# Performance work log

Hardware: AMD Instinct MI355X
Metric: run time of the kernel (lower is better)

Reference implementation:

```python
import jax, jax.numpy as jnp
import numpy as np

B, D, E, H = 8192, 2048, 8, 128

def setup_inputs() -> dict:
    key = jax.random.key(0)
    ks = jax.random.split(key, 9)
    s_d = 1.0 / np.sqrt(D)
    s_h = 1.0 / np.sqrt(H)
    return {
        "x": jax.random.normal(ks[0], (B, D), dtype=jnp.float32),
        "gate_w": jax.random.normal(ks[1], (D, E), dtype=jnp.float32) * s_d,
        "gate_b": jnp.zeros((E,), dtype=jnp.float32),
        "W1": jax.random.normal(ks[2], (E, D, H), dtype=jnp.float32) * s_d,
        "b1": jnp.zeros((E, H), dtype=jnp.float32),
        "W2": jax.random.normal(ks[3], (E, H, H), dtype=jnp.float32) * s_h,
        "b2": jnp.zeros((E, H), dtype=jnp.float32),
        "W3": jax.random.normal(ks[4], (E, H, D), dtype=jnp.float32) * s_h,
        "b3": jnp.zeros((E, D), dtype=jnp.float32),
    }

def reference(x, gate_w, gate_b, W1, b1, W2, b2, W3, b3):
    # Adaptive gate: softmax over experts
    gates = jax.nn.softmax(x @ gate_w + gate_b, axis=1)          # [B, E]
    # All experts as one batched (grouped) GEMM over the expert axis.
    h1 = jax.nn.silu(jnp.einsum('bd,edh->ebh', x, W1) + b1[:, None, :])   # [E, B, H]
    h2 = jax.nn.silu(jnp.einsum('ebh,ehk->ebk', h1, W2) + b2[:, None, :]) # [E, B, H]
    y = jnp.einsum('ebh,ehd->ebd', h2, W3) + b3[:, None, :]               # [E, B, D]
    # Gate-weighted sum over experts (fused reduction, no [B,E,D] stack kept)
    out = jnp.einsum('be,ebd->bd', gates, y)                     # [B, D]
    return out
```

## Files before the change

kernel.cpp:

```cpp
#include <hip/hip_runtime.h>


typedef __attribute__((ext_vector_type(8))) short short8;
typedef __attribute__((ext_vector_type(4))) float f32x4;

#define B_SZ 8192
#define D_SZ 2048
#define E_SZ 8
#define H_SZ 128

#define VMCNT(n) asm volatile("s_waitcnt vmcnt(" #n ")" ::: "memory")
#define BAR()    __builtin_amdgcn_s_barrier()

__device__ __forceinline__ short f2bf(float f) {
  unsigned u = __builtin_bit_cast(unsigned, f);
  unsigned r = (u + 0x7fffu + ((u >> 16) & 1u)) >> 16;
  return (short)r;
}

__device__ __forceinline__ float silu_f(float v) {
  return v / (1.f + __expf(-v));
}

__device__ __forceinline__ void gload_lds16(const void* g, void* l) {
  __builtin_amdgcn_global_load_lds(
      (const __attribute__((address_space(1))) void*)g,
      (__attribute__((address_space(3))) void*)l,
      16, 0, 0);
}

__global__ __launch_bounds__(256)
void k_convert(const float* __restrict__ x,  const float* __restrict__ W1,
               const float* __restrict__ W2, const float* __restrict__ W3,
               short* __restrict__ xf, short* __restrict__ w1f,
               short* __restrict__ w2f, short* __restrict__ w3f)
{
  const int gi = blockIdx.x * 256 + threadIdx.x;
  if (gi < 2097152) {
    const int t = gi >> 10, r = gi & 1023;
    const int bt = t >> 5, kt = t & 31;
    const int kg = r >> 7, p = r & 127;
    const float* src = x + (size_t)(bt*128 + p)*2048 + kt*64 + kg*8;
    const float4 v0 = *(const float4*)src;
    const float4 v1 = *(const float4*)(src + 4);
    short8 o;
    o[0]=f2bf(v0.x); o[1]=f2bf(v0.y); o[2]=f2bf(v0.z); o[3]=f2bf(v0.w);
    o[4]=f2bf(v1.x); o[5]=f2bf(v1.y); o[6]=f2bf(v1.z); o[7]=f2bf(v1.w);
    *(short8*)(xf + (size_t)gi*8) = o;
  } else if (gi < 2097152 + 262144) {
    const int g = gi - 2097152;
    const int t = g >> 10, r = g & 1023;
    const int e = t >> 5, kt = t & 31;
    const int kg = r >> 7, p = r & 127;
    const int k0 = kt*64 + kg*8;
    short8 o;
    #pragma unroll
    for (int j = 0; j < 8; ++j)
      o[j] = f2bf(W1[(size_t)e*262144 + (size_t)(k0 + j)*128 + p]);
    *(short8*)(w1f + (size_t)g*8) = o;
  } else if (gi < 2097152 + 262144 + 16384) {
    const int g = gi - (2097152 + 262144);
    const int t = g >> 10, r = g & 1023;
    const int e = t >> 1, kt = t & 1;
    const int kg = r >> 7, p = r & 127;
    const int k0 = kt*64 + kg*8;
    short8 o;
    #pragma unroll
    for (int j = 0; j < 8; ++j)
      o[j] = f2bf(W2[(size_t)e*16384 + (size_t)(k0 + j)*128 + p]);
    *(short8*)(w2f + (size_t)g*8) = o;
  } else if (gi < 2637824) {
    const int g = gi - 2375680;
    const int t = g >> 10, r = g & 1023;
    const int nt = t >> 4, kt = t & 15;
    const int kg = r >> 7, p = r & 127;
    const int k0 = kt*64 + kg*8;
    short8 o;
    #pragma unroll
    for (int j = 0; j < 8; ++j) {
      const int k = k0 + j;
      o[j] = f2bf(W3[(size_t)(k >> 7)*262144 + (size_t)(k & 127)*2048 + nt*128 + p]);
    }
    *(short8*)(w3f + (size_t)g*8) = o;
  }
}

__global__ __launch_bounds__(256)
void k_gate(const float* __restrict__ x, const float* __restrict__ gw,
            const float* __restrict__ gb, float* __restrict__ gates)
{
  const int wid = threadIdx.x >> 6, lane = threadIdx.x & 63;
  const int row = blockIdx.x * 4 + wid;
  const float* xr = x + (size_t)row * 2048;
  float acc[8] = {0.f,0.f,0.f,0.f,0.f,0.f,0.f,0.f};
  for (int it = 0; it < 32; ++it) {
    const int k = it*64 + lane;
    const float xv = xr[k];
    const float4 g0 = *(const float4*)(gw + (size_t)k*8);
    const float4 g1 = *(const float4*)(gw + (size_t)k*8 + 4);
    acc[0] += xv*g0.x; acc[1] += xv*g0.y; acc[2] += xv*g0.z; acc[3] += xv*g0.w;
    acc[4] += xv*g1.x; acc[5] += xv*g1.y; acc[6] += xv*g1.z; acc[7] += xv*g1.w;
  }
  #pragma unroll
  for (int e = 0; e < 8; ++e) {
    #pragma unroll
    for (int d = 1; d < 64; d <<= 1)
      acc[e] += __shfl_xor(acc[e], d, 64);
  }
  if (lane == 0) {
    float lg[8], mx = -1e30f;
    #pragma unroll
    for (int e = 0; e < 8; ++e) { lg[e] = acc[e] + gb[e]; mx = fmaxf(mx, lg[e]); }
    float s = 0.f;
    #pragma unroll
    for (int e = 0; e < 8; ++e) { lg[e] = __expf(lg[e] - mx); s += lg[e]; }
    const float inv = 1.f / s;
    #pragma unroll
    for (int e = 0; e < 8; ++e) gates[(size_t)row*8 + e] = lg[e] * inv;
  }
}

__global__ __launch_bounds__(512, 2)
void k_gemm12(const short* __restrict__ xf, const short* __restrict__ w1f,
              const short* __restrict__ w2f,
              const float* __restrict__ b1, const float* __restrict__ b2,
              const float* __restrict__ gates, short* __restrict__ h2gf)
{
  __shared__ short lds[65536];
  const int wg = blockIdx.x;
  const int xcd = wg & 7, idx = wg >> 3;
  const int bt = xcd*8 + (idx >> 2);
  const int nt = idx & 3;

  const int tid  = threadIdx.x;
  const int lane = tid & 63;
  const int wid  = tid >> 6;
  const int wm = wid >> 2, wn = wid & 3;
  const int lm = lane & 15, lk = lane >> 4, lr = lane >> 4;
  const int wlds = (tid & ~63) * 8;

  const short* Ab  = xf + (size_t)bt*32*8192;
  const short* Bb0 = w1f + (size_t)(2*nt)*32*8192;
  const short* Bb1 = w1f + (size_t)(2*nt+1)*32*8192;

  f32x4 acc[4][4] = {};

  auto STAGE = [&](int n2) {
    const int tau = n2 >> 1, ks = n2 & 1, b = tau & 1;
    gload_lds16(Ab  + (size_t)tau*8192 + ks*4096 + tid*8,
                lds + b*24576 + ks*4096 + wlds);
    gload_lds16(Bb0 + (size_t)tau*8192 + ks*4096 + tid*8,
                lds + b*24576 + 8192 + ks*4096 + wlds);
    gload_lds16(Bb1 + (size_t)tau*8192 + ks*4096 + tid*8,
                lds + b*24576 + 16384 + ks*4096 + wlds);
  };

  STAGE(0); STAGE(1);
  VMCNT(3); BAR();

  for (int n = 0; n < 64; ++n) {
    const int tau = n >> 1, ks = n & 1, b = tau & 1;
    if (n + 2 < 64) STAGE(n + 2);
    short8 av[4], bv[4];
    #pragma unroll
    for (int f = 0; f < 4; ++f)
      av[f] = *(const short8*)(lds + b*24576 + (ks*4+lk)*1024 + (wm*64 + f*16 + lm)*8);
    #pragma unroll
    for (int f = 0; f < 4; ++f)
      bv[f] = *(const short8*)(lds + b*24576 + 8192 + (wn>>1)*8192 + (ks*4+lk)*1024
                               + ((wn&1)*64 + f*16 + lm)*8);
    #pragma unroll
    for (int i = 0; i < 4; ++i)
      #pragma unroll
      for (int j = 0; j < 4; ++j)
        acc[i][j] = __builtin_amdgcn_mfma_f32_16x16x32_bf16(av[i], bv[j], acc[i][j], 0, 0, 0);
    if (n + 2 < 64)      { VMCNT(3); BAR(); }
    else if (n + 1 < 64) { VMCNT(0); BAR(); }
  }
  BAR();

  #pragma unroll
  for (int q = 0; q < 8; ++q)
    gload_lds16(w2f + (size_t)nt*32768 + q*4096 + tid*8, lds + 32768 + q*4096 + wlds);

  float b1v[4];
  #pragma unroll
  for (int fn = 0; fn < 4; ++fn) b1v[fn] = b1[nt*256 + wn*64 + fn*16 + lm];
  #pragma unroll
  for (int fm = 0; fm < 4; ++fm)
  #pragma unroll
  for (int i = 0; i < 4; ++i) {
    const int m = wm*64 + fm*16 + lr*4 + i;
    #pragma unroll
    for (int fn = 0; fn < 4; ++fn) {
      const int n = wn*64 + fn*16 + lm;
      const float v = silu_f(acc[fm][fn][i] + b1v[fn]);
      lds[(n>>7)*16384 + ((n>>6)&1)*8192 + ((n>>3)&7)*1024 + m*8 + (n&7)] = f2bf(v);
    }
  }
  VMCNT(0); BAR();

  const int wm2 = wid >> 2, wn2 = wid & 3;
  #pragma unroll
  for (int eh = 0; eh < 2; ++eh) {
    f32x4 acc2[4][2] = {};
    #pragma unroll
    for (int kt2 = 0; kt2 < 2; ++kt2)
    #pragma unroll
    for (int ks = 0; ks < 2; ++ks) {
      short8 a2[4], b2v[2];
      #pragma unroll
      for (int f = 0; f < 4; ++f)
        a2[f] = *(const short8*)(lds + eh*16384 + kt2*8192 + (ks*4+lk)*1024
                                 + (wm2*64 + f*16 + lm)*8);
      #pragma unroll
      for (int f = 0; f < 2; ++f)
        b2v[f] = *(const short8*)(lds + 32768 + eh*16384 + kt2*8192 + (ks*4+lk)*1024
                                  + (wn2*32 + f*16 + lm)*8);
      #pragma unroll
      for (int i = 0; i < 4; ++i)
        #pragma unroll
        for (int j = 0; j < 2; ++j)
          acc2[i][j] = __builtin_amdgcn_mfma_f32_16x16x32_bf16(a2[i], b2v[j], acc2[i][j], 0, 0, 0);
    }
    BAR();

    const int e = 2*nt + eh;
    #pragma unroll
    for (int fm = 0; fm < 4; ++fm)
    #pragma unroll
    for (int i = 0; i < 4; ++i) {
      const int m = wm2*64 + fm*16 + lr*4 + i;
      const float g = gates[(size_t)(bt*128 + m)*8 + e];
      #pragma unroll
      for (int fn = 0; fn < 2; ++fn) {
        const int h = wn2*32 + fn*16 + lm;
        const float v = silu_f(acc2[fm][fn][i] + b2[e*128 + h]) * g;
        lds[32768 + ((h>>6)&1)*8192 + ((h>>3)&7)*1024 + m*8 + (h&7)] = f2bf(v);
      }
    }
    BAR();
    #pragma unroll
    for (int q = 0; q < 4; ++q) {
      const int li = q*4096 + tid*8;
      const int t2 = li >> 13, o = li & 8191;
      *(short8*)(h2gf + ((size_t)bt*16 + 2*e + t2)*8192 + o) =
          *(const short8*)(lds + 32768 + li);
    }
    if (eh == 0) BAR();
  }
}

__global__ __launch_bounds__(512, 2)
void k_gemm3(const short* __restrict__ h2gf, const short* __restrict__ w3f,
             const float* __restrict__ b3, const float* __restrict__ gates,
             float* __restrict__ out)
{
  __shared__ short lds[65536];
  const int wg = blockIdx.x;
  const int xcd = wg & 7, idx = wg >> 3;
  const int bt = xcd*4 + (idx & 3);
  const int nt = idx >> 2;

  const int tid  = threadIdx.x;
  const int lane = tid & 63;
  const int wid  = tid >> 6;
  const int wm = wid >> 2, wn = wid & 3;
  const int lm = lane & 15, lk = lane >> 4, lr = lane >> 4;
  const int wlds = (tid & ~63) * 8;

  const short* A0 = h2gf + (size_t)(bt*2)*16*8192;
  const short* A1 = h2gf + (size_t)(bt*2+1)*16*8192;
  const short* B0 = w3f + (size_t)(2*nt)*16*8192;
  const short* B1 = w3f + (size_t)(2*nt+1)*16*8192;

  f32x4 acc[8][4] = {};

  auto STAGE = [&](int n2) {
    const int tau = n2 >> 1, ks = n2 & 1, b = tau & 1;
    gload_lds16(A0 + (size_t)tau*8192 + ks*4096 + tid*8,
                lds + b*32768 + ks*4096 + wlds);
    gload_lds16(A1 + (size_t)tau*8192 + ks*4096 + tid*8,
                lds + b*32768 + 8192 + ks*4096 + wlds);
    gload_lds16(B0 + (size_t)tau*8192 + ks*4096 + tid*8,
                lds + b*32768 + 16384 + ks*4096 + wlds);
    gload_lds16(B1 + (size_t)tau*8192 + ks*4096 + tid*8,
                lds + b*32768 + 24576 + ks*4096 + wlds);
  };

  STAGE(0); STAGE(1);
  VMCNT(4); BAR();

  for (int n = 0; n < 32; ++n) {
    const int tau = n >> 1, ks = n & 1, b = tau & 1;
    if (n + 2 < 32) STAGE(n + 2);
    short8 av[8], bv[4];
    #pragma unroll
    for (int f = 0; f < 8; ++f)
      av[f] = *(const short8*)(lds + b*32768 + wm*8192 + (ks*4+lk)*1024 + (f*16 + lm)*8);
    #pragma unroll
    for (int f = 0; f < 4; ++f)
      bv[f] = *(const short8*)(lds + b*32768 + 16384 + (wn>>1)*8192 + (ks*4+lk)*1024
                               + ((wn&1)*64 + f*16 + lm)*8);
    #pragma unroll
    for (int i = 0; i < 8; ++i)
      #pragma unroll
      for (int j = 0; j < 4; ++j)
        acc[i][j] = __builtin_amdgcn_mfma_f32_16x16x32_bf16(av[i], bv[j], acc[i][j], 0, 0, 0);
    if (n + 2 < 32)      { VMCNT(4); BAR(); }
    else if (n + 1 < 32) { VMCNT(0); BAR(); }
  }

  float b3c[4][8];
  #pragma unroll
  for (int fn = 0; fn < 4; ++fn) {
    const int n = nt*256 + wn*64 + fn*16 + lm;
    #pragma unroll
    for (int e = 0; e < 8; ++e) b3c[fn][e] = b3[(size_t)e*D_SZ + n];
  }
  #pragma unroll
  for (int fm = 0; fm < 8; ++fm)
  #pragma unroll
  for (int i = 0; i < 4; ++i) {
    const int m = bt*256 + wm*128 + fm*16 + lr*4 + i;
    const float4 ga  = *(const float4*)(gates + (size_t)m*8);
    const float4 gbv = *(const float4*)(gates + (size_t)m*8 + 4);
    #pragma unroll
    for (int fn = 0; fn < 4; ++fn) {
      const int n = nt*256 + wn*64 + fn*16 + lm;
      const float bias = ga.x*b3c[fn][0] + ga.y*b3c[fn][1] + ga.z*b3c[fn][2] + ga.w*b3c[fn][3]
                       + gbv.x*b3c[fn][4] + gbv.y*b3c[fn][5] + gbv.z*b3c[fn][6] + gbv.w*b3c[fn][7];
      out[(size_t)m*D_SZ + n] = acc[fm][fn][i] + bias;
    }
  }
}

extern "C" void kernel_launch(void* const* d_in, const int* in_sizes, int n_in,
                              void* d_out, int out_size, void* d_ws, size_t ws_size,
                              hipStream_t stream)
{
  (void)in_sizes; (void)n_in; (void)out_size; (void)ws_size;
  const float* x  = (const float*)d_in[0];
  const float* gw = (const float*)d_in[1];
  const float* gb = (const float*)d_in[2];
  const float* W1 = (const float*)d_in[3];
  const float* b1 = (const float*)d_in[4];
  const float* W2 = (const float*)d_in[5];
  const float* b2 = (const float*)d_in[6];
  const float* W3 = (const float*)d_in[7];
  const float* b3 = (const float*)d_in[8];
  float* out = (float*)d_out;

  char* ws = (char*)d_ws;
  short* xf    = (short*)ws;  ws += (size_t)B_SZ*D_SZ*2;
  short* w1f   = (short*)ws;  ws += (size_t)E_SZ*D_SZ*H_SZ*2;
  short* w2f   = (short*)ws;  ws += (size_t)E_SZ*H_SZ*H_SZ*2;
  short* w3f   = (short*)ws;  ws += (size_t)E_SZ*H_SZ*D_SZ*2;
  float* gates = (float*)ws;  ws += (size_t)B_SZ*E_SZ*4;
  short* h2gf  = (short*)ws;  ws += (size_t)B_SZ*E_SZ*H_SZ*2;

  k_convert<<<dim3(10304), dim3(256), 0, stream>>>(x, W1, W2, W3, xf, w1f, w2f, w3f);
  k_gate   <<<dim3(2048),  dim3(256), 0, stream>>>(x, gw, gb, gates);
  k_gemm12 <<<dim3(256), dim3(512), 0, stream>>>(xf, w1f, w2f, b1, b2, gates, h2gf);
  k_gemm3  <<<dim3(256), dim3(512), 0, stream>>>(h2gf, w3f, b3, gates, out);
}
```

Measured before the change: 141.1 us.

## Split first GEMM into split-K 256x256 tiles and separate second-layer kernel

The fused GEMM1+GEMM2 kernel is replaced by a split-K GEMM1 kernel that uses a shared 256x256 tile core, writing two bf16 partial sums to a workspace. A new kernel then adds the partials, applies bias and SiLU, and runs the per-expert 128x128 GEMM2 with gating. The larger tile is meant to raise data reuse, and the split-K is meant to keep the grid at 256 blocks. In exchange it adds an extra launch and a round trip of partial sums through global memory, which also loses precision because the partials are rounded to bf16. MFMA sections are additionally wrapped in s_setprio.

After: 150.8 us. +6.9%, slower.

```diff
diff --git a/kernel.cpp b/kernel.cpp
--- a/kernel.cpp
+++ b/kernel.cpp
@@ -16,6 +16,10 @@
   unsigned u = __builtin_bit_cast(unsigned, f);
   unsigned r = (u + 0x7fffu + ((u >> 16) & 1u)) >> 16;
   return (short)r;
+}
+
+__device__ __forceinline__ float bf2f(short s) {
+  return __builtin_bit_cast(float, (unsigned)((unsigned short)s) << 16);
 }
 
 __device__ __forceinline__ float silu_f(float v) {
@@ -27,6 +31,58 @@
       (const __attribute__((address_space(1))) void*)g,
       (__attribute__((address_space(3))) void*)l,
       16, 0, 0);
+}
+
+template<int NKT>
+__device__ __forceinline__ void core256(const short* __restrict__ A0,
+                                        const short* __restrict__ A1,
+                                        const short* __restrict__ B0,
+                                        const short* __restrict__ B1,
+                                        short* lds, f32x4 acc[8][4])
+{
+  const int tid  = threadIdx.x;
+  const int lane = tid & 63;
+  const int wid  = tid >> 6;
+  const int wm = wid >> 2, wn = wid & 3;
+  const int lm = lane & 15, lk = lane >> 4;
+  const int wlds = (tid & ~63) * 8;
+
+  auto STAGE = [&](int n2) {
+    const int tau = n2 >> 1, ks = n2 & 1, b = tau & 1;
+    gload_lds16(A0 + (size_t)tau*8192 + ks*4096 + tid*8,
+                lds + b*32768 + ks*4096 + wlds);
+    gload_lds16(A1 + (size_t)tau*8192 + ks*4096 + tid*8,
+                lds + b*32768 + 8192 + ks*4096 + wlds);
+    gload_lds16(B0 + (size_t)tau*8192 + ks*4096 + tid*8,
+                lds + b*32768 + 16384 + ks*4096 + wlds);
+    gload_lds16(B1 + (size_t)tau*8192 + ks*4096 + tid*8,
+                lds + b*32768 + 24576 + ks*4096 + wlds);
+  };
+
+  STAGE(0); STAGE(1);
+  VMCNT(4); BAR();
+
+  for (int n = 0; n < 2*NKT; ++n) {
+    const int ks = n & 1, b = (n >> 1) & 1;
+    if (n + 2 < 2*NKT) STAGE(n + 2);
+    short8 av[8], bv[4];
+    #pragma unroll
+    for (int f = 0; f < 8; ++f)
+      av[f] = *(const short8*)(lds + b*32768 + wm*8192 + (ks*4+lk)*1024 + (f*16 + lm)*8);
+    #pragma unroll
+    for (int f = 0; f < 4; ++f)
+      bv[f] = *(const short8*)(lds + b*32768 + 16384 + (wn>>1)*8192 + (ks*4+lk)*1024
+                               + ((wn&1)*64 + f*16 + lm)*8);
+    __builtin_amdgcn_s_setprio(1);
+    #pragma unroll
+    for (int i = 0; i < 8; ++i)
+      #pragma unroll
+      for (int j = 0; j < 4; ++j)
+        acc[i][j] = __builtin_amdgcn_mfma_f32_16x16x32_bf16(av[i], bv[j], acc[i][j], 0, 0, 0);
+    __builtin_amdgcn_s_setprio(0);
+    if (n + 2 < 2*NKT)      { VMCNT(4); BAR(); }
+    else if (n + 1 < 2*NKT) { VMCNT(0); BAR(); }
+  }
 }
 
 __global__ __launch_bounds__(256)
@@ -121,133 +177,115 @@
 }
 
 __global__ __launch_bounds__(512, 2)
-void k_gemm12(const short* __restrict__ xf, const short* __restrict__ w1f,
-              const short* __restrict__ w2f,
+void k_gemm1s(const short* __restrict__ xf, const short* __restrict__ w1f,
+              short* __restrict__ p)
+{
+  __shared__ short lds[65536];
+  const int b = blockIdx.x;
+  const int xcd = b & 7, idx = b >> 3;
+  const int BT = xcd*4 + (idx >> 3);
+  const int rem = idx & 7;
+  const int NT = rem >> 1, kh = rem & 1;
+
+  f32x4 acc[8][4] = {};
+  core256<16>(xf  + ((size_t)(BT*2)  *32 + kh*16)*8192,
+              xf  + ((size_t)(BT*2+1)*32 + kh*16)*8192,
+              w1f + ((size_t)(2*NT)  *32 + kh*16)*8192,
+              w1f + ((size_t)(2*NT+1)*32 + kh*16)*8192,
+              lds, acc);
+
+  const int tid = threadIdx.x, lane = tid & 63, wid = tid >> 6;
+  const int wm = wid >> 2, wn = wid & 3, lm = lane & 15, lr = lane >> 4;
+  short* pd = p + (size_t)kh*8388608;
+  #pragma unroll
+  for (int fm = 0; fm < 8; ++fm)
+  #pragma unroll
+  for (int i = 0; i < 4; ++i) {
+    const int m = BT*256 + wm*128 + fm*16 + lr*4 + i;
+    #pragma unroll
+    for (int fn = 0; fn < 4; ++fn) {
+      const int n = NT*256 + wn*64 + fn*16 + lm;
+      pd[(size_t)m*1024 + n] = f2bf(acc[fm][fn][i]);
+    }
+  }
+}
+
+__global__ __launch_bounds__(256, 2)
+void k_gemm2m(const short* __restrict__ p, const short* __restrict__ w2f,
               const float* __restrict__ b1, const float* __restrict__ b2,
               const float* __restrict__ gates, short* __restrict__ h2gf)
 {
-  __shared__ short lds[65536];
-  const int wg = blockIdx.x;
-  const int xcd = wg & 7, idx = wg >> 3;
-  const int bt = xcd*8 + (idx >> 2);
-  const int nt = idx & 3;
-
-  const int tid  = threadIdx.x;
-  const int lane = tid & 63;
-  const int wid  = tid >> 6;
-  const int wm = wid >> 2, wn = wid & 3;
-  const int lm = lane & 15, lk = lane >> 4, lr = lane >> 4;
+  __shared__ short lds[32768];
+  const int bt2 = blockIdx.x, e = blockIdx.y;
+  const int tid = threadIdx.x;
   const int wlds = (tid & ~63) * 8;
 
-  const short* Ab  = xf + (size_t)bt*32*8192;
-  const short* Bb0 = w1f + (size_t)(2*nt)*32*8192;
-  const short* Bb1 = w1f + (size_t)(2*nt+1)*32*8192;
-
+  #pragma unroll
+  for (int q = 0; q < 8; ++q)
+    gload_lds16(w2f + (size_t)e*16384 + q*2048 + tid*8,
+                lds + 16384 + q*2048 + wlds);
+
+  #pragma unroll
+  for (int u = 0; u < 8; ++u) {
+    const int g = u*256 + tid;
+    const int m = g >> 4, hg = g & 15;
+    const size_t src = (size_t)(bt2*128 + m)*1024 + e*128 + hg*8;
+    const short8 a = *(const short8*)(p + src);
+    const short8 c = *(const short8*)(p + 8388608 + src);
+    short8 o;
+    #pragma unroll
+    for (int j = 0; j < 8; ++j) {
+      const float v = bf2f(a[j]) + bf2f(c[j]) + b1[e*128 + hg*8 + j];
+      o[j] = f2bf(silu_f(v));
+    }
+    *(short8*)(lds + (hg>>3)*8192 + (hg&7)*1024 + m*8) = o;
+  }
+  VMCNT(0);
+  __syncthreads();
+
+  const int lane = tid & 63, wid = tid >> 6;
+  const int wr = wid >> 1, wc = wid & 1, lm = lane & 15, lk = lane >> 4, lr = lane >> 4;
   f32x4 acc[4][4] = {};
-
-  auto STAGE = [&](int n2) {
-    const int tau = n2 >> 1, ks = n2 & 1, b = tau & 1;
-    gload_lds16(Ab  + (size_t)tau*8192 + ks*4096 + tid*8,
-                lds + b*24576 + ks*4096 + wlds);
-    gload_lds16(Bb0 + (size_t)tau*8192 + ks*4096 + tid*8,
-                lds + b*24576 + 8192 + ks*4096 + wlds);
-    gload_lds16(Bb1 + (size_t)tau*8192 + ks*4096 + tid*8,
-                lds + b*24576 + 16384 + ks*4096 + wlds);
-  };
-
-  STAGE(0); STAGE(1);
-  VMCNT(3); BAR();
-
-  for (int n = 0; n < 64; ++n) {
-    const int tau = n >> 1, ks = n & 1, b = tau & 1;
-    if (n + 2 < 64) STAGE(n + 2);
+  #pragma unroll
+  for (int kt = 0; kt < 2; ++kt)
+  #pragma unroll
+  for (int ks = 0; ks < 2; ++ks) {
     short8 av[4], bv[4];
     #pragma unroll
     for (int f = 0; f < 4; ++f)
-      av[f] = *(const short8*)(lds + b*24576 + (ks*4+lk)*1024 + (wm*64 + f*16 + lm)*8);
+      av[f] = *(const short8*)(lds + kt*8192 + (ks*4+lk)*1024 + (wr*64 + f*16 + lm)*8);
     #pragma unroll
     for (int f = 0; f < 4; ++f)
-      bv[f] = *(const short8*)(lds + b*24576 + 8192 + (wn>>1)*8192 + (ks*4+lk)*1024
-                               + ((wn&1)*64 + f*16 + lm)*8);
+      bv[f] = *(const short8*)(lds + 16384 + kt*8192 + (ks*4+lk)*1024 + (wc*64 + f*16 + lm)*8);
     #pragma unroll
     for (int i = 0; i < 4; ++i)
       #pragma unroll
       for (int j = 0; j < 4; ++j)
         acc[i][j] = __builtin_amdgcn_mfma_f32_16x16x32_bf16(av[i], bv[j], acc[i][j], 0, 0, 0);
-    if (n + 2 < 64)      { VMCNT(3); BAR(); }
-    else if (n + 1 < 64) { VMCNT(0); BAR(); }
-  }
-  BAR();
-
-  #pragma unroll
-  for (int q = 0; q < 8; ++q)
-    gload_lds16(w2f + (size_t)nt*32768 + q*4096 + tid*8, lds + 32768 + q*4096 + wlds);
-
-  float b1v[4];
-  #pragma unroll
-  for (int fn = 0; fn < 4; ++fn) b1v[fn] = b1[nt*256 + wn*64 + fn*16 + lm];
+  }
+  __syncthreads();
+
   #pragma unroll
   for (int fm = 0; fm < 4; ++fm)
   #pragma unroll
   for (int i = 0; i < 4; ++i) {
-    const int m = wm*64 + fm*16 + lr*4 + i;
+    const int m = wr*64 + fm*16 + lr*4 + i;
+    const float g = gates[(size_t)(bt2*128 + m)*8 + e];
     #pragma unroll
     for (int fn = 0; fn < 4; ++fn) {
-      const int n = wn*64 + fn*16 + lm;
-      const float v = silu_f(acc[fm][fn][i] + b1v[fn]);
-      lds[(n>>7)*16384 + ((n>>6)&1)*8192 + ((n>>3)&7)*1024 + m*8 + (n&7)] = f2bf(v);
-    }
-  }
-  VMCNT(0); BAR();
-
-  const int wm2 = wid >> 2, wn2 = wid & 3;
-  #pragma unroll
-  for (int eh = 0; eh < 2; ++eh) {
-    f32x4 acc2[4][2] = {};
-    #pragma unroll
-    for (int kt2 = 0; kt2 < 2; ++kt2)
-    #pragma unroll
-    for (int ks = 0; ks < 2; ++ks) {
-      short8 a2[4], b2v[2];
-      #pragma unroll
-      for (int f = 0; f < 4; ++f)
-        a2[f] = *(const short8*)(lds + eh*16384 + kt2*8192 + (ks*4+lk)*1024
-                                 + (wm2*64 + f*16 + lm)*8);
-      #pragma unroll
-      for (int f = 0; f < 2; ++f)
-        b2v[f] = *(const short8*)(lds + 32768 + eh*16384 + kt2*8192 + (ks*4+lk)*1024
-                                  + (wn2*32 + f*16 + lm)*8);
-      #pragma unroll
-      for (int i = 0; i < 4; ++i)
-        #pragma unroll
-        for (int j = 0; j < 2; ++j)
-          acc2[i][j] = __builtin_amdgcn_mfma_f32_16x16x32_bf16(a2[i], b2v[j], acc2[i][j], 0, 0, 0);
-    }
-    BAR();
-
-    const int e = 2*nt + eh;
-    #pragma unroll
-    for (int fm = 0; fm < 4; ++fm)
-    #pragma unroll
-    for (int i = 0; i < 4; ++i) {
-      const int m = wm2*64 + fm*16 + lr*4 + i;
-      const float g = gates[(size_t)(bt*128 + m)*8 + e];
-      #pragma unroll
-      for (int fn = 0; fn < 2; ++fn) {
-        const int h = wn2*32 + fn*16 + lm;
-        const float v = silu_f(acc2[fm][fn][i] + b2[e*128 + h]) * g;
-        lds[32768 + ((h>>6)&1)*8192 + ((h>>3)&7)*1024 + m*8 + (h&7)] = f2bf(v);
-      }
-    }
-    BAR();
-    #pragma unroll
-    for (int q = 0; q < 4; ++q) {
-      const int li = q*4096 + tid*8;
-      const int t2 = li >> 13, o = li & 8191;
-      *(short8*)(h2gf + ((size_t)bt*16 + 2*e + t2)*8192 + o) =
-          *(const short8*)(lds + 32768 + li);
-    }
-    if (eh == 0) BAR();
+      const int h = wc*64 + fn*16 + lm;
+      const float v = silu_f(acc[fm][fn][i] + b2[e*128 + h]) * g;
+      lds[(h>>6)*8192 + ((h>>3)&7)*1024 + m*8 + (h&7)] = f2bf(v);
+    }
+  }
+  __syncthreads();
+
+  #pragma unroll
+  for (int q = 0; q < 8; ++q) {
+    const int g = q*256 + tid;
+    const int li = g*8;
+    const int t2 = li >> 13, o = li & 8191;
+    *(short8*)(h2gf + ((size_t)bt2*16 + e*2 + t2)*8192 + o) = *(const short8*)(lds + li);
   }
 }
 
@@ -262,55 +300,15 @@
   const int bt = xcd*4 + (idx & 3);
   const int nt = idx >> 2;
 
-  const int tid  = threadIdx.x;
-  const int lane = tid & 63;
-  const int wid  = tid >> 6;
-  const int wm = wid >> 2, wn = wid & 3;
-  const int lm = lane & 15, lk = lane >> 4, lr = lane >> 4;
-  const int wlds = (tid & ~63) * 8;
-
-  const short* A0 = h2gf + (size_t)(bt*2)*16*8192;
-  const short* A1 = h2gf + (size_t)(bt*2+1)*16*8192;
-  const short* B0 = w3f + (size_t)(2*nt)*16*8192;
-  const short* B1 = w3f + (size_t)(2*nt+1)*16*8192;
-
   f32x4 acc[8][4] = {};
-
-  auto STAGE = [&](int n2) {
-    const int tau = n2 >> 1, ks = n2 & 1, b = tau & 1;
-    gload_lds16(A0 + (size_t)tau*8192 + ks*4096 + tid*8,
-                lds + b*32768 + ks*4096 + wlds);
-    gload_lds16(A1 + (size_t)tau*8192 + ks*4096 + tid*8,
-                lds + b*32768 + 8192 + ks*4096 + wlds);
-    gload_lds16(B0 + (size_t)tau*8192 + ks*4096 + tid*8,
-                lds + b*32768 + 16384 + ks*4096 + wlds);
-    gload_lds16(B1 + (size_t)tau*8192 + ks*4096 + tid*8,
-                lds + b*32768 + 24576 + ks*4096 + wlds);
-  };
-
-  STAGE(0); STAGE(1);
-  VMCNT(4); BAR();
-
-  for (int n = 0; n < 32; ++n) {
-    const int tau = n >> 1, ks = n & 1, b = tau & 1;
-    if (n + 2 < 32) STAGE(n + 2);
-    short8 av[8], bv[4];
-    #pragma unroll
-    for (int f = 0; f < 8; ++f)
-      av[f] = *(const short8*)(lds + b*32768 + wm*8192 + (ks*4+lk)*1024 + (f*16 + lm)*8);
-    #pragma unroll
-    for (int f = 0; f < 4; ++f)
-      bv[f] = *(const short8*)(lds + b*32768 + 16384 + (wn>>1)*8192 + (ks*4+lk)*1024
-                               + ((wn&1)*64 + f*16 + lm)*8);
-    #pragma unroll
-    for (int i = 0; i < 8; ++i)
-      #pragma unroll
-      for (int j = 0; j < 4; ++j)
-        acc[i][j] = __builtin_amdgcn_mfma_f32_16x16x32_bf16(av[i], bv[j], acc[i][j], 0, 0, 0);
-    if (n + 2 < 32)      { VMCNT(4); BAR(); }
-    else if (n + 1 < 32) { VMCNT(0); BAR(); }
-  }
-
+  core256<16>(h2gf + (size_t)(bt*2)  *16*8192,
+              h2gf + (size_t)(bt*2+1)*16*8192,
+              w3f  + (size_t)(2*nt)  *16*8192,
+              w3f  + (size_t)(2*nt+1)*16*8192,
+              lds, acc);
+
+  const int tid = threadIdx.x, lane = tid & 63, wid = tid >> 6;
+  const int wm = wid >> 2, wn = wid & 3, lm = lane & 15, lr = lane >> 4;
   float b3c[4][8];
   #pragma unroll
   for (int fn = 0; fn < 4; ++fn) {
@@ -357,10 +355,12 @@
   short* w2f   = (short*)ws;  ws += (size_t)E_SZ*H_SZ*H_SZ*2;
   short* w3f   = (short*)ws;  ws += (size_t)E_SZ*H_SZ*D_SZ*2;
   float* gates = (float*)ws;  ws += (size_t)B_SZ*E_SZ*4;
+  short* p     = (short*)ws;  ws += (size_t)2*B_SZ*1024*2;
   short* h2gf  = (short*)ws;  ws += (size_t)B_SZ*E_SZ*H_SZ*2;
 
   k_convert<<<dim3(10304), dim3(256), 0, stream>>>(x, W1, W2, W3, xf, w1f, w2f, w3f);
   k_gate   <<<dim3(2048),  dim3(256), 0, stream>>>(x, gw, gb, gates);
-  k_gemm12 <<<dim3(256), dim3(512), 0, stream>>>(xf, w1f, w2f, b1, b2, gates, h2gf);
-  k_gemm3  <<<dim3(256), dim3(512), 0, stream>>>(h2gf, w3f, b3, gates, out);
-}
+  k_gemm1s <<<dim3(256),   dim3(512), 0, stream>>>(xf, w1f, p);
+  k_gemm2m <<<dim3(64, 8), dim3(256), 0, stream>>>(p, w2f, b1, b2, gates, h2gf);
+  k_gemm3  <<<dim3(256),   dim3(512), 0, stream>>>(h2gf, w3f, b3, gates, out);
+}
```
